# Performance work log

Measured on AMD Instinct MI355X. Metric: run time of the kernel, lower is better.

## Reference

```python
import jax, jax.numpy as jnp
import numpy as np

INPUT_SIZE = 1024
HIDDEN_SIZE = 1024
LN_EPS = 1e-5


def setup_inputs() -> dict:
    key = jax.random.key(0)
    ks = jax.random.split(key, 8)
    bs, n = 4, 2048
    # Xavier-uniform bound for square (in=out) linear layers
    bound = float(np.sqrt(6.0 / (INPUT_SIZE + HIDDEN_SIZE)))
    x = jax.random.normal(ks[0], (bs, n, INPUT_SIZE), dtype=jnp.float32)
    wq = jax.random.uniform(ks[1], (INPUT_SIZE, HIDDEN_SIZE), jnp.float32, -bound, bound)
    wk = jax.random.uniform(ks[2], (INPUT_SIZE, HIDDEN_SIZE), jnp.float32, -bound, bound)
    wv = jax.random.uniform(ks[3], (INPUT_SIZE, HIDDEN_SIZE), jnp.float32, -bound, bound)
    bq = jnp.zeros((HIDDEN_SIZE,), jnp.float32)
    bk = jnp.zeros((HIDDEN_SIZE,), jnp.float32)
    bv = jnp.zeros((HIDDEN_SIZE,), jnp.float32)
    ln_w = jnp.ones((INPUT_SIZE,), jnp.float32)
    ln_b = jnp.zeros((INPUT_SIZE,), jnp.float32)
    return {"x": x, "wq": wq, "bq": bq, "wk": wk, "bk": bk,
            "wv": wv, "bv": bv, "ln_w": ln_w, "ln_b": ln_b}


def _layernorm(x, w, b):
    mu = jnp.mean(x, axis=-1, keepdims=True)
    var = jnp.mean(jnp.square(x - mu), axis=-1, keepdims=True)
    return (x - mu) * jax.lax.rsqrt(var + LN_EPS) * w + b


def reference(x, wq, bq, wk, bk, wv, bv, ln_w, ln_b):
    # x: [b, n, d_in]
    xn = _layernorm(x, ln_w, ln_b)
    q = jnp.einsum('bnd,dh->bnh', xn, wq) + bq
    k = jnp.einsum('bnd,dh->bnh', xn, wk) + bk
    v = jnp.einsum('bnd,dh->bnh', xn, wv) + bv
    scale = 1.0 / np.sqrt(HIDDEN_SIZE)
    att = jnp.einsum('bqh,bkh->bqk', q, k) * scale  # [b, n, n]
    att = jax.nn.softmax(att, axis=-1)
    out = jnp.einsum('bqk,bkh->bqh', att, v)  # [b, n, h]
    return (att, out)
```

## Files before the change

### kernel.cpp

```cpp
#include <hip/hip_runtime.h>
#include <stdint.h>


typedef __attribute__((ext_vector_type(8))) short short8;
typedef __attribute__((ext_vector_type(4))) float floatx4;
typedef __attribute__((ext_vector_type(4))) uint16_t u16x4;

__device__ __forceinline__ uint16_t f2bf(float f) {
    union { float f; uint32_t u; } v; v.f = f;
    uint32_t r = v.u + 0x7fffu + ((v.u >> 16) & 1u);
    return (uint16_t)(r >> 16);
}

typedef const uint32_t __attribute__((address_space(1)))* gas1_t;
typedef uint32_t __attribute__((address_space(3)))* las3_t;
__device__ __forceinline__ void gload_lds16(const uint16_t* g, uint16_t* l) {
    __builtin_amdgcn_global_load_lds((gas1_t)g, (las3_t)l, 16, 0, 0);
}

__device__ __forceinline__ void s_bar()  { asm volatile("s_barrier" ::: "memory"); }
__device__ __forceinline__ void lgkm0()  { asm volatile("s_waitcnt lgkmcnt(0)" ::: "memory"); }
template<int N> __device__ __forceinline__ void vmw() {
    asm volatile("s_waitcnt vmcnt(%0)" :: "n"(N) : "memory");
}


#define RA(MF, MI)                                                        \
    { Af[(MF)][0] = *(const short8*)(LA + aoff + (MI) * 1024 + ksg0);     \
      Af[(MF)][1] = *(const short8*)(LA + aoff + (MI) * 1024 + ksg1); }
#define RB(NI)                                                            \
    { Bf[(NI)][0] = *(const short8*)(LB + boff + (NI) * 1024 + ksg0);     \
      Bf[(NI)][1] = *(const short8*)(LB + boff + (NI) * 1024 + ksg1); }
#define CLUST(MA, MF, NI0)                                                \
    __builtin_amdgcn_s_setprio(1);                                        \
    _Pragma("unroll") for (int mi = 0; mi < 4; ++mi)                      \
    _Pragma("unroll") for (int nn = 0; nn < 2; ++nn)                      \
    _Pragma("unroll") for (int ks = 0; ks < 2; ++ks)                      \
        acc[(MA) + mi][(NI0) + nn] =                                      \
            __builtin_amdgcn_mfma_f32_16x16x32_bf16(                      \
                Af[(MF) + mi][ks], Bf[(NI0) + nn][ks],                    \
                acc[(MA) + mi][(NI0) + nn], 0, 0, 0);                     \
    __builtin_amdgcn_s_setprio(0);
#define CLUST1(NI)                                                        \
    __builtin_amdgcn_s_setprio(1);                                        \
    _Pragma("unroll") for (int mi = 0; mi < 8; ++mi)                      \
    _Pragma("unroll") for (int ks = 0; ks < 2; ++ks)                      \
        acc[mi][(NI)] = __builtin_amdgcn_mfma_f32_16x16x32_bf16(          \
            Af[mi][ks], Bf[(NI)][ks], acc[mi][(NI)], 0, 0, 0);            \
    __builtin_amdgcn_s_setprio(0);

template<int BN, int EPI>
__device__ __forceinline__ void gemm8p(
    const uint16_t* __restrict__ A, const uint16_t* __restrict__ Bt,
    const int K, const int NT, const int m0, const int n0,
    float* __restrict__ Cf, uint16_t* __restrict__ Cb, const int ldc,
    const float* __restrict__ bq, const float* __restrict__ bk,
    const float* __restrict__ bv, const float alpha)
{
    constexpr int ABUF  = 256 * 64;
    constexpr int BP    = BN / 64;
    constexpr int BBUF  = BN * 64;
    constexpr int BUFSZ = ABUF + BBUF;
    constexpr int NIW   = BN / 64;
    constexpr int OPS   = 4 + BP;
    constexpr int NBUF  = (BN == 128) ? 3 : 2;
    __shared__ uint16_t sm[NBUF * BUFSZ + 4096];
    uint16_t* const trash = sm + NBUF * BUFSZ;

    const int t = threadIdx.x;

    const int srow = t >> 3;
    const int sseg = (t & 7) ^ (srow & 7);
    const uint16_t* gA = A + (size_t)(m0 + srow) * K + sseg * 8;
    const uint16_t* gB = Bt + (size_t)(n0 + srow) * K + sseg * 8;

    auto STGALL = [&](int kt, int bi) {
        const int live = kt < NT;
        const size_t ko = (size_t)(live ? kt : 0) * 64;
        uint16_t* const db = sm + bi * BUFSZ + t * 8;
        uint16_t* const tr = trash + t * 8;
#pragma unroll
        for (int p = 0; p < 4; ++p)
            gload_lds16(gA + (size_t)(p * 64) * K + ko,
                        live ? (db + p * 4096) : tr);
#pragma unroll
        for (int p = 0; p < BP; ++p)
            gload_lds16(gB + (size_t)(p * 64) * K + ko,
                        live ? (db + ABUF + p * 4096) : tr);
    };

    const int lane = t & 63;
    const int wid  = t >> 6;
    const int wm   = wid >> 2;
    const int wn   = wid & 3;
    const int quad = lane >> 4;
    const int lrow = lane & 15;
    const int swz  = lrow & 7;
    const int ksg0 = (quad ^ swz) * 8;
    const int ksg1 = ((4 + quad) ^ swz) * 8;
    const int aoff = (wm * 128 + lrow) * 64;
    const int boff = (wn * (16 * NIW) + lrow) * 64;

    floatx4 acc[8][NIW];
#pragma unroll
    for (int mi = 0; mi < 8; ++mi)
#pragma unroll
        for (int ni = 0; ni < NIW; ++ni)
            acc[mi][ni] = floatx4{0.f, 0.f, 0.f, 0.f};

    short8 Af[(BN == 192) ? 8 : 4][2];
    short8 Bf[NIW][2];

    STGALL(0, 0);
    STGALL(1, 1);
    vmw<OPS>();
    s_bar();

    int bcur = 0, bstage = 2;
    for (int te = 0; te < NT; ++te) {
        const int bi = (BN == 128) ? bcur : (te & 1);
        const uint16_t* LA = sm + bi * BUFSZ;
        const uint16_t* LB = LA + ABUF;

        if constexpr (BN == 256) {
            RA(0, 0) RA(1, 1) RA(2, 2) RA(3, 3) RB(0) RB(1)
            s_bar(); lgkm0();
            CLUST(0, 0, 0)
            s_bar();
            RB(2) RB(3)
            s_bar(); lgkm0();
            CLUST(0, 0, 2)
            s_bar();
            RA(0, 4) RA(1, 5) RA(2, 6) RA(3, 7)
            s_bar(); lgkm0();
            CLUST(4, 0, 0)
            s_bar();
            STGALL(te + 2, bi);
            s_bar();
            CLUST(4, 0, 2)
            vmw<OPS>();
            s_bar();
        } else if constexpr (BN == 192) {
            RA(0, 0) RA(1, 1) RA(2, 2) RA(3, 3) RB(0) RB(1)
            s_bar(); lgkm0();
            CLUST(0, 0, 0)
            s_bar();
            RA(4, 4) RA(5, 5) RA(6, 6) RA(7, 7) RB(2)
            s_bar(); lgkm0();
            CLUST(4, 4, 0)
            s_bar();
            STGALL(te + 2, bi);
            s_bar();
            CLUST1(2)
            vmw<OPS>();
            s_bar();
        } else {
            STGALL(te + 2, bstage);
            RA(0, 0) RA(1, 1) RA(2, 2) RA(3, 3) RB(0) RB(1)
            s_bar(); lgkm0();
            CLUST(0, 0, 0)
            s_bar();
            RA(0, 4) RA(1, 5) RA(2, 6) RA(3, 7)
            s_bar(); lgkm0();
            CLUST(4, 0, 0)
            vmw<OPS>();
            s_bar();
            bcur   = (bcur == 2) ? 0 : bcur + 1;
            bstage = (bstage == 2) ? 0 : bstage + 1;
        }
    }

    vmw<0>();

    const int rbase = m0 + wm * 128 + quad * 4;
    const int cbase = n0 + wn * (16 * NIW) + lrow;

    if constexpr (EPI == 1) {
        float bc[NIW];
#pragma unroll
        for (int ni = 0; ni < NIW; ++ni) {
            const int col = cbase + ni * 16;
            const int z = col >> 10;
            const float* bp = (z == 0) ? bq : ((z == 1) ? bk : bv);
            bc[ni] = bp[col & 1023];
        }
#pragma unroll
        for (int mi = 0; mi < 8; ++mi) {
#pragma unroll
            for (int ni = 0; ni < NIW; ++ni) {
                const int row = rbase + mi * 16;
                const int col = cbase + ni * 16;
                const int z = col >> 10, h = col & 1023;
#pragma unroll
                for (int r = 0; r < 4; ++r)
                    Cb[(size_t)z * 8388608 + (size_t)(row + r) * 1024 + h] =
                        f2bf(acc[mi][ni][r] + bc[ni]);
            }
        }
    } else {
#pragma unroll
        for (int mi = 0; mi < 8; ++mi) {
#pragma unroll
            for (int ni = 0; ni < NIW; ++ni) {
                const int row = rbase + mi * 16;
                const int col = cbase + ni * 16;
#pragma unroll
                for (int r = 0; r < 4; ++r)
                    Cf[(size_t)(row + r) * ldc + col] = acc[mi][ni][r] * alpha;
            }
        }
    }
}

__global__ __launch_bounds__(512, 2) void k_qkv(
    const uint16_t* __restrict__ xn, const uint16_t* __restrict__ wt,
    const float* __restrict__ bq, const float* __restrict__ bk,
    const float* __restrict__ bv, uint16_t* __restrict__ qkv)
{
    const int flat = blockIdx.y * 16 + blockIdx.x;
    const int s = (flat & 7) * 64 + (flat >> 3);
    const int bx = s & 15, by = s >> 4;
    gemm8p<192, 1>(xn, wt, 1024, 16, by * 256, bx * 192,
                   nullptr, qkv, 0, bq, bk, bv, 0.f);
}

__global__ __launch_bounds__(512, 2) void k_scores(
    const uint16_t* __restrict__ q, const uint16_t* __restrict__ k,
    float* __restrict__ S)
{
    const int flat = blockIdx.z * 64 + blockIdx.y * 8 + blockIdx.x;
    const int s = (flat & 7) * 32 + (flat >> 3);
    const int z = s >> 6, y = (s >> 3) & 7, x = s & 7;
    gemm8p<256, 0>(q + (size_t)z * 2048 * 1024, k + (size_t)z * 2048 * 1024,
                   1024, 16, y * 256, x * 256,
                   S + (size_t)z * 2048 * 2048, nullptr, 2048,
                   nullptr, nullptr, nullptr, 0.03125f);
}

__global__ __launch_bounds__(512, 2) void k_out(
    const uint16_t* __restrict__ attb, const uint16_t* __restrict__ vt,
    float* __restrict__ out)
{
    const int flat = blockIdx.z * 64 + blockIdx.y * 8 + blockIdx.x;
    const int s = (flat & 7) * 32 + (flat >> 3);
    const int z = s >> 6, y = (s >> 3) & 7, x = s & 7;
    gemm8p<128, 0>(attb + (size_t)z * 2048 * 2048, vt + (size_t)z * 1024 * 2048,
                   2048, 32, y * 256, x * 128,
                   out + (size_t)z * 2048 * 1024, nullptr, 1024,
                   nullptr, nullptr, nullptr, 1.0f);
}

__global__ __launch_bounds__(256) void k_ln(
    const float* __restrict__ x, const float* __restrict__ lw,
    const float* __restrict__ lb, uint16_t* __restrict__ xn)
{
    const int row = blockIdx.x;
    const int t = threadIdx.x;
    const float* xr = x + (size_t)row * 1024;
    const float4 xv = ((const float4*)xr)[t];
    float s  = xv.x + xv.y + xv.z + xv.w;
    float s2 = xv.x * xv.x + xv.y * xv.y + xv.z * xv.z + xv.w * xv.w;
#pragma unroll
    for (int off = 32; off > 0; off >>= 1) {
        s  += __shfl_xor(s, off);
        s2 += __shfl_xor(s2, off);
    }
    __shared__ float ps[4], ps2[4];
    const int w = t >> 6, lane = t & 63;
    if (lane == 0) { ps[w] = s; ps2[w] = s2; }
    __syncthreads();
    s  = ps[0] + ps[1] + ps[2] + ps[3];
    s2 = ps2[0] + ps2[1] + ps2[2] + ps2[3];
    const float mu  = s * (1.f / 1024.f);
    const float var = s2 * (1.f / 1024.f) - mu * mu;
    const float rs  = rsqrtf(var + 1e-5f);
    const float4 wv = ((const float4*)lw)[t];
    const float4 bv = ((const float4*)lb)[t];
    u16x4 o;
    o.x = f2bf((xv.x - mu) * rs * wv.x + bv.x);
    o.y = f2bf((xv.y - mu) * rs * wv.y + bv.y);
    o.z = f2bf((xv.z - mu) * rs * wv.z + bv.z);
    o.w = f2bf((xv.w - mu) * rs * wv.w + bv.w);
    ((u16x4*)(xn + (size_t)row * 1024))[t] = o;
}

__global__ void k_wt(const float* __restrict__ wq, const float* __restrict__ wk,
                     const float* __restrict__ wv, uint16_t* __restrict__ wt)
{
    __shared__ float tile[32][33];
    const int z = blockIdx.z;
    const float* W = (z == 0) ? wq : ((z == 1) ? wk : wv);
    uint16_t* T = wt + (size_t)z * 1024 * 1024;
    const int c0 = blockIdx.x * 32, r0 = blockIdx.y * 32;
    const int tx = threadIdx.x, ty = threadIdx.y;
#pragma unroll
    for (int i = 0; i < 4; i++)
        tile[ty + 8 * i][tx] = W[(size_t)(r0 + ty + 8 * i) * 1024 + c0 + tx];
    __syncthreads();
#pragma unroll
    for (int i = 0; i < 4; i++)
        T[(size_t)(c0 + ty + 8 * i) * 1024 + r0 + tx] = f2bf(tile[tx][ty + 8 * i]);
}

__global__ __launch_bounds__(256) void k_vt(
    const uint16_t* __restrict__ v, uint16_t* __restrict__ vt)
{
    __shared__ uint16_t tile[64][68];
    const int b = blockIdx.z;
    const uint16_t* V = v + (size_t)b * 2048 * 1024;
    uint16_t* T = vt + (size_t)b * 1024 * 2048;
    const int h0 = blockIdx.x * 64, t0 = blockIdx.y * 64;
    const int t = threadIdx.x;
    const int rr = t >> 4;
    const int cc = (t & 15) * 4;
#pragma unroll
    for (int i = 0; i < 4; i++) {
        const int tok = rr + 16 * i;
        *(u16x4*)&tile[tok][cc] =
            *(const u16x4*)&V[(size_t)(t0 + tok) * 1024 + h0 + cc];
    }
    __syncthreads();
#pragma unroll
    for (int i = 0; i < 4; i++) {
        const int h = rr + 16 * i;
        u16x4 o;
        o.x = tile[cc + 0][h];
        o.y = tile[cc + 1][h];
        o.z = tile[cc + 2][h];
        o.w = tile[cc + 3][h];
        *(u16x4*)&T[(size_t)(h0 + h) * 2048 + t0 + cc] = o;
    }
}

__global__ __launch_bounds__(256) void k_softmax(
    float* __restrict__ S, uint16_t* __restrict__ attb)
{
    const size_t row = blockIdx.x;
    float* p = S + row * 2048;
    const int t = threadIdx.x;
    float4 a = ((float4*)p)[2 * t];
    float4 b = ((float4*)p)[2 * t + 1];
    float m = fmaxf(fmaxf(fmaxf(a.x, a.y), fmaxf(a.z, a.w)),
                    fmaxf(fmaxf(b.x, b.y), fmaxf(b.z, b.w)));
#pragma unroll
    for (int off = 32; off > 0; off >>= 1) m = fmaxf(m, __shfl_xor(m, off));
    __shared__ float pm[4], pl[4];
    const int w = t >> 6, lane = t & 63;
    if (lane == 0) pm[w] = m;
    __syncthreads();
    m = fmaxf(fmaxf(pm[0], pm[1]), fmaxf(pm[2], pm[3]));

    a.x = __expf(a.x - m); a.y = __expf(a.y - m);
    a.z = __expf(a.z - m); a.w = __expf(a.w - m);
    b.x = __expf(b.x - m); b.y = __expf(b.y - m);
    b.z = __expf(b.z - m); b.w = __expf(b.w - m);
    float s = a.x + a.y + a.z + a.w + b.x + b.y + b.z + b.w;
#pragma unroll
    for (int off = 32; off > 0; off >>= 1) s += __shfl_xor(s, off);
    if (lane == 0) pl[w] = s;
    __syncthreads();
    s = pl[0] + pl[1] + pl[2] + pl[3];
    const float inv = 1.f / s;

    a.x *= inv; a.y *= inv; a.z *= inv; a.w *= inv;
    b.x *= inv; b.y *= inv; b.z *= inv; b.w *= inv;
    ((float4*)p)[2 * t]     = a;
    ((float4*)p)[2 * t + 1] = b;

    uint16_t* q = attb + row * 2048 + t * 8;
    u16x4 o0, o1;
    o0.x = f2bf(a.x); o0.y = f2bf(a.y); o0.z = f2bf(a.z); o0.w = f2bf(a.w);
    o1.x = f2bf(b.x); o1.y = f2bf(b.y); o1.z = f2bf(b.z); o1.w = f2bf(b.w);
    ((u16x4*)q)[0] = o0;
    ((u16x4*)q)[1] = o1;
}

extern "C" void kernel_launch(void* const* d_in, const int* in_sizes, int n_in,
                              void* d_out, int out_size, void* d_ws, size_t ws_size,
                              hipStream_t stream)
{
    const float* x  = (const float*)d_in[0];
    const float* wq = (const float*)d_in[1];
    const float* bq = (const float*)d_in[2];
    const float* wk = (const float*)d_in[3];
    const float* bk = (const float*)d_in[4];
    const float* wv = (const float*)d_in[5];
    const float* bv = (const float*)d_in[6];
    const float* lw = (const float*)d_in[7];
    const float* lb = (const float*)d_in[8];

    float* att = (float*)d_out;
    float* out = (float*)d_out + (size_t)16777216;

    uint16_t* xn = (uint16_t*)d_out;
    uint16_t* wt = (uint16_t*)d_out + (size_t)8388608;

    uint16_t* ws   = (uint16_t*)d_ws;
    uint16_t* q    = ws;
    uint16_t* k    = ws + (size_t)8388608;
    uint16_t* v    = ws + (size_t)2 * 8388608;
    uint16_t* vt   = ws;
    uint16_t* attb = ws + (size_t)8388608;
    uint16_t* qkv  = q;

    if (ws_size < (size_t)50331648) return;

    k_ln<<<8192, 256, 0, stream>>>(x, lw, lb, xn);
    k_wt<<<dim3(32, 32, 3), dim3(32, 8), 0, stream>>>(wq, wk, wv, wt);
    k_qkv<<<dim3(16, 32), 512, 0, stream>>>(xn, wt, bq, bk, bv, qkv);
    k_scores<<<dim3(8, 8, 4), 512, 0, stream>>>(q, k, att);
    k_vt<<<dim3(16, 32, 4), 256, 0, stream>>>(v, vt);
    k_softmax<<<8192, 256, 0, stream>>>(att, attb);
    k_out<<<dim3(8, 8, 4), 512, 0, stream>>>(attb, vt, out);
}
```

Baseline: 314.7 us.

## Remove intra-iteration barriers in GEMM core and re-tile BN=128 waves as 4x2

Replaces the ping-pong barrier schedule inside each K-step, where waves alternated LDS reads and MFMA clusters across several s_barrier points, with a single lgkm wait and barrier per phase. Fragment reads are issued back-to-back and the MFMAs run without intermediate waits, leaving the compiler to insert the needed waits. For BN=128, the wave layout changes from 2x4 to 4x2 so each wave computes a 64x64 tile, reading the A and B fragments once per step. Dropping the barrier-staged interleaving may cost some overlap between waves and raises register pressure from holding more fragments at once.

```diff
diff --git a/kernel.cpp b/kernel.cpp
--- a/kernel.cpp
+++ b/kernel.cpp
@@ -50,7 +50,7 @@
     __builtin_amdgcn_s_setprio(0);
 
 template<int BN, int EPI>
-__device__ __forceinline__ void gemm8p(
+__device__ __forceinline__ void gemm_core(
     const uint16_t* __restrict__ A, const uint16_t* __restrict__ Bt,
     const int K, const int NT, const int m0, const int n0,
     float* __restrict__ Cf, uint16_t* __restrict__ Cb, const int ldc,
@@ -61,9 +61,12 @@
     constexpr int BP    = BN / 64;
     constexpr int BBUF  = BN * 64;
     constexpr int BUFSZ = ABUF + BBUF;
-    constexpr int NIW   = BN / 64;
     constexpr int OPS   = 4 + BP;
     constexpr int NBUF  = (BN == 128) ? 3 : 2;
+    constexpr int WAVES_N = (BN == 128) ? 2 : 4;
+    constexpr int MIW  = (BN == 128) ? 4 : 8;
+    constexpr int NIW  = BN / (16 * WAVES_N);
+    constexpr int NFR  = (BN == 256) ? 4 : MIW;
     __shared__ uint16_t sm[NBUF * BUFSZ + 4096];
     uint16_t* const trash = sm + NBUF * BUFSZ;
 
@@ -91,24 +94,24 @@
 
     const int lane = t & 63;
     const int wid  = t >> 6;
-    const int wm   = wid >> 2;
-    const int wn   = wid & 3;
+    const int wm   = wid / WAVES_N;
+    const int wn   = wid % WAVES_N;
     const int quad = lane >> 4;
     const int lrow = lane & 15;
     const int swz  = lrow & 7;
     const int ksg0 = (quad ^ swz) * 8;
     const int ksg1 = ((4 + quad) ^ swz) * 8;
-    const int aoff = (wm * 128 + lrow) * 64;
+    const int aoff = (wm * (16 * MIW) + lrow) * 64;
     const int boff = (wn * (16 * NIW) + lrow) * 64;
 
-    floatx4 acc[8][NIW];
-#pragma unroll
-    for (int mi = 0; mi < 8; ++mi)
+    floatx4 acc[MIW][NIW];
+#pragma unroll
+    for (int mi = 0; mi < MIW; ++mi)
 #pragma unroll
         for (int ni = 0; ni < NIW; ++ni)
             acc[mi][ni] = floatx4{0.f, 0.f, 0.f, 0.f};
 
-    short8 Af[(BN == 192) ? 8 : 4][2];
+    short8 Af[NFR][2];
     short8 Bf[NIW][2];
 
     STGALL(0, 0);
@@ -123,48 +126,30 @@
         const uint16_t* LB = LA + ABUF;
 
         if constexpr (BN == 256) {
-            RA(0, 0) RA(1, 1) RA(2, 2) RA(3, 3) RB(0) RB(1)
-            s_bar(); lgkm0();
-            CLUST(0, 0, 0)
-            s_bar();
-            RB(2) RB(3)
-            s_bar(); lgkm0();
-            CLUST(0, 0, 2)
-            s_bar();
+            RA(0, 0) RA(1, 1) RA(2, 2) RA(3, 3)
+            RB(0) RB(1) RB(2) RB(3)
+            CLUST(0, 0, 0) CLUST(0, 0, 2)
             RA(0, 4) RA(1, 5) RA(2, 6) RA(3, 7)
-            s_bar(); lgkm0();
-            CLUST(4, 0, 0)
-            s_bar();
+            lgkm0(); s_bar();
             STGALL(te + 2, bi);
-            s_bar();
-            CLUST(4, 0, 2)
-            vmw<OPS>();
-            s_bar();
+            CLUST(4, 0, 0) CLUST(4, 0, 2)
+            vmw<OPS>(); s_bar();
         } else if constexpr (BN == 192) {
-            RA(0, 0) RA(1, 1) RA(2, 2) RA(3, 3) RB(0) RB(1)
-            s_bar(); lgkm0();
-            CLUST(0, 0, 0)
-            s_bar();
-            RA(4, 4) RA(5, 5) RA(6, 6) RA(7, 7) RB(2)
-            s_bar(); lgkm0();
-            CLUST(4, 4, 0)
-            s_bar();
+            RA(0, 0) RA(1, 1) RA(2, 2) RA(3, 3)
+            RA(4, 4) RA(5, 5) RA(6, 6) RA(7, 7)
+            RB(0) RB(1) RB(2)
+            CLUST(0, 0, 0) CLUST(4, 4, 0)
+            lgkm0(); s_bar();
             STGALL(te + 2, bi);
-            s_bar();
             CLUST1(2)
-            vmw<OPS>();
-            s_bar();
+            vmw<OPS>(); s_bar();
         } else {
             STGALL(te + 2, bstage);
-            RA(0, 0) RA(1, 1) RA(2, 2) RA(3, 3) RB(0) RB(1)
-            s_bar(); lgkm0();
-            CLUST(0, 0, 0)
-            s_bar();
-            RA(0, 4) RA(1, 5) RA(2, 6) RA(3, 7)
-            s_bar(); lgkm0();
-            CLUST(4, 0, 0)
-            vmw<OPS>();
-            s_bar();
+            RA(0, 0) RA(1, 1) RA(2, 2) RA(3, 3)
+            RB(0) RB(1) RB(2) RB(3)
+            CLUST(0, 0, 0) CLUST(0, 0, 2)
+            lgkm0();
+            vmw<OPS>(); s_bar();
             bcur   = (bcur == 2) ? 0 : bcur + 1;
             bstage = (bstage == 2) ? 0 : bstage + 1;
         }
@@ -172,7 +157,7 @@
 
     vmw<0>();
 
-    const int rbase = m0 + wm * 128 + quad * 4;
+    const int rbase = m0 + wm * (16 * MIW) + quad * 4;
     const int cbase = n0 + wn * (16 * NIW) + lrow;
 
     if constexpr (EPI == 1) {
@@ -185,7 +170,7 @@
             bc[ni] = bp[col & 1023];
         }
 #pragma unroll
-        for (int mi = 0; mi < 8; ++mi) {
+        for (int mi = 0; mi < MIW; ++mi) {
 #pragma unroll
             for (int ni = 0; ni < NIW; ++ni) {
                 const int row = rbase + mi * 16;
@@ -199,7 +184,7 @@
         }
     } else {
 #pragma unroll
-        for (int mi = 0; mi < 8; ++mi) {
+        for (int mi = 0; mi < MIW; ++mi) {
 #pragma unroll
             for (int ni = 0; ni < NIW; ++ni) {
                 const int row = rbase + mi * 16;
@@ -220,8 +205,8 @@
     const int flat = blockIdx.y * 16 + blockIdx.x;
     const int s = (flat & 7) * 64 + (flat >> 3);
     const int bx = s & 15, by = s >> 4;
-    gemm8p<192, 1>(xn, wt, 1024, 16, by * 256, bx * 192,
-                   nullptr, qkv, 0, bq, bk, bv, 0.f);
+    gemm_core<192, 1>(xn, wt, 1024, 16, by * 256, bx * 192,
+                      nullptr, qkv, 0, bq, bk, bv, 0.f);
 }
 
 __global__ __launch_bounds__(512, 2) void k_scores(
@@ -231,10 +216,10 @@
     const int flat = blockIdx.z * 64 + blockIdx.y * 8 + blockIdx.x;
     const int s = (flat & 7) * 32 + (flat >> 3);
     const int z = s >> 6, y = (s >> 3) & 7, x = s & 7;
-    gemm8p<256, 0>(q + (size_t)z * 2048 * 1024, k + (size_t)z * 2048 * 1024,
-                   1024, 16, y * 256, x * 256,
-                   S + (size_t)z * 2048 * 2048, nullptr, 2048,
-                   nullptr, nullptr, nullptr, 0.03125f);
+    gemm_core<256, 0>(q + (size_t)z * 2048 * 1024, k + (size_t)z * 2048 * 1024,
+                      1024, 16, y * 256, x * 256,
+                      S + (size_t)z * 2048 * 2048, nullptr, 2048,
+                      nullptr, nullptr, nullptr, 0.03125f);
 }
 
 __global__ __launch_bounds__(512, 2) void k_out(
@@ -244,10 +229,10 @@
     const int flat = blockIdx.z * 64 + blockIdx.y * 8 + blockIdx.x;
     const int s = (flat & 7) * 32 + (flat >> 3);
     const int z = s >> 6, y = (s >> 3) & 7, x = s & 7;
-    gemm8p<128, 0>(attb + (size_t)z * 2048 * 2048, vt + (size_t)z * 1024 * 2048,
-                   2048, 32, y * 256, x * 128,
-                   out + (size_t)z * 2048 * 1024, nullptr, 1024,
-                   nullptr, nullptr, nullptr, 1.0f);
+    gemm_core<128, 0>(attb + (size_t)z * 2048 * 2048, vt + (size_t)z * 1024 * 2048,
+                      2048, 32, y * 256, x * 128,
+                      out + (size_t)z * 2048 * 1024, nullptr, 1024,
+                      nullptr, nullptr, nullptr, 1.0f);
 }
 
 __global__ __launch_bounds__(256) void k_ln(
```

Result: faster. 307.3 us (-2.4%).
